# Optimization experiments

Measured on AMD Instinct MI355X. Metric: run time of the kernel, lower is better.

The kernel has to match this reference:

```python
import jax, jax.numpy as jnp
import numpy as np
import math

B, T, Dm, H = 512, 64, 1024, 16
dh = Dm // H
CD, SD = 32, 256  # smolgen compress_dim, shared_dim
SCALE = 1.0 / math.sqrt(dh)
RES_SCALE = 1.0 / math.sqrt(2.0)  # n_layers=1
EPS = 1e-5


def _ln(v, g, b):
    m = jnp.mean(v, axis=-1, keepdims=True)
    var = jnp.mean(jnp.square(v - m), axis=-1, keepdims=True)
    return (v - m) * jax.lax.rsqrt(var + EPS) * g + b


def setup_inputs() -> dict:
    key = jax.random.key(0)
    ks = jax.random.split(key, 16)
    s = 0.02
    return {
        "x": jax.random.normal(ks[0], (B, T, Dm), jnp.float32),
        # weights stored (in, out); y = x @ W + b
        "Wq": jax.random.normal(ks[1], (Dm, Dm), jnp.float32) * s,
        "Wk": jax.random.normal(ks[2], (Dm, Dm), jnp.float32) * s,
        "Wv": jax.random.normal(ks[3], (Dm, Dm), jnp.float32) * s,
        "Wo_w": jax.random.normal(ks[4], (Dm, Dm), jnp.float32) * s,
        "Wo_b": jnp.zeros((Dm,), jnp.float32),
        "static_bias": jax.random.normal(ks[5], (H, T, T), jnp.float32) * s,
        "aQ": jax.random.normal(ks[6], (H, T, T, dh), jnp.float32) * s,
        "aK": jax.random.normal(ks[7], (H, T, T, dh), jnp.float32) * s,
        "aV": jax.random.normal(ks[8], (H, T, T, dh), jnp.float32) * s,
        # Smolgen params
        "pt_w": jax.random.normal(ks[9], (Dm, CD), jnp.float32) * s,
        "pt_b": jnp.zeros((CD,), jnp.float32),
        "pg_w": jax.random.normal(ks[10], (T * CD, SD), jnp.float32) * s,
        "pg_b": jnp.zeros((SD,), jnp.float32),
        "ph_w": jax.random.normal(ks[11], (SD, H * SD), jnp.float32) * s,
        "ph_b": jnp.zeros((H * SD,), jnp.float32),
        "ln1_g": jnp.ones((SD,), jnp.float32),
        "ln1_b": jnp.zeros((SD,), jnp.float32),
        "ln2_g": jnp.ones((SD,), jnp.float32),
        "ln2_b": jnp.zeros((SD,), jnp.float32),
        "shared_w": jax.random.normal(ks[12], (SD, T * T), jnp.float32) * s,
    }


def _smolgen(x, pt_w, pt_b, pg_w, pg_b, ph_w, ph_b, ln1_g, ln1_b, ln2_g, ln2_b, shared_w):
    z = x @ pt_w + pt_b                      # (B,T,CD)
    g = z.reshape(x.shape[0], T * CD) @ pg_w + pg_b  # (B,SD)
    g = _ln(jax.nn.silu(g), ln1_g, ln1_b)
    u = g @ ph_w + ph_b                      # (B,H*SD)
    u = jax.nn.silu(u).reshape(-1, H, SD)
    u = _ln(u, ln2_g, ln2_b)
    return (u @ shared_w).reshape(-1, H, T, T)


def reference(x, Wq, Wk, Wv, Wo_w, Wo_b, static_bias, aQ, aK, aV,
              pt_w, pt_b, pg_w, pg_b, ph_w, ph_b,
              ln1_g, ln1_b, ln2_g, ln2_b, shared_w):
    Bx = x.shape[0]
    Q = (x @ Wq).reshape(Bx, T, H, dh).transpose(0, 2, 1, 3)  # (B,H,T,dh)
    K = (x @ Wk).reshape(Bx, T, H, dh).transpose(0, 2, 1, 3)
    V = (x @ Wv).reshape(Bx, T, H, dh).transpose(0, 2, 1, 3)
    logits = jnp.einsum('bhtd,bhsd->bhts', Q, K) * SCALE
    logits = logits + static_bias[None]
    logits = logits + jnp.einsum('bhtd,htsd->bhts', Q, aK) * SCALE
    logits = logits + jnp.einsum('htsd,bhsd->bhts', aQ, K) * SCALE
    logits = logits + (jnp.einsum('htsd,htsd->hts', aQ, aK) * SCALE)[None]
    logits = logits + _smolgen(x, pt_w, pt_b, pg_w, pg_b, ph_w, ph_b,
                               ln1_g, ln1_b, ln2_g, ln2_b, shared_w)
    attn = jax.nn.softmax(logits, axis=-1)  # dropout = identity (eval mode)
    out = jnp.einsum('bhts,bhsd->bhtd', attn, V)
    out = out + jnp.einsum('bhts,htsd->bhtd', attn, aV)
    out = out.transpose(0, 2, 1, 3).reshape(Bx, T, Dm)
    return (out @ Wo_w + Wo_b) * RES_SCALE
```

## Files before the change

### kernel.cpp

```cpp
#include <hip/hip_runtime.h>
#include <cstdint>
#include <cstdio>

typedef unsigned short u16;
typedef __attribute__((ext_vector_type(8))) short s8v;
typedef __attribute__((ext_vector_type(4))) float f4v;
typedef __attribute__((ext_vector_type(4))) unsigned short u16x4;
typedef const __attribute__((address_space(1))) void* gas_p;
typedef __attribute__((address_space(3))) void* las_p;

#define DEV __device__ __forceinline__

static constexpr float SCALE_ = 0.125f;
static constexpr float RES_SCALE_ = 0.7071067811865475f;
static constexpr float EPS_ = 1e-5f;

DEV u16 f2bf(float f) {
  uint32_t u = __float_as_uint(f);
  u += 0x7fffu + ((u >> 16) & 1u);
  return (u16)(u >> 16);
}
DEV float bf2f(u16 h) { return __uint_as_float(((uint32_t)h) << 16); }

DEV f4v mfma16(s8v a, s8v b, f4v c) {
  return __builtin_amdgcn_mfma_f32_16x16x32_bf16(a, b, c, 0, 0, 0);
}

#define WAITVM4 asm volatile("s_waitcnt vmcnt(4)" ::: "memory")
#define WAITVM0 asm volatile("s_waitcnt vmcnt(0)" ::: "memory")
#define SCHEDB  __builtin_amdgcn_sched_barrier(0)
#define BAR     __builtin_amdgcn_s_barrier()


__global__ void k_zero(float* __restrict__ p, long n) {
  long i = (long)blockIdx.x * blockDim.x + threadIdx.x;
  long stride = (long)gridDim.x * blockDim.x;
  for (; i < n; i += stride) p[i] = 0.f;
}

__global__ void k_cvt(const float* __restrict__ in, u16* __restrict__ out, long n4) {
  long i = (long)blockIdx.x * blockDim.x + threadIdx.x;
  long stride = (long)gridDim.x * blockDim.x;
  for (; i < n4; i += stride) {
    f4v v = *(const f4v*)&in[i * 4];
    u16x4 o;
    o.x = f2bf(v.x); o.y = f2bf(v.y); o.z = f2bf(v.z); o.w = f2bf(v.w);
    *(u16x4*)&out[i * 4] = o;
  }
}

__global__ void k_transpose(const float* __restrict__ in, u16* __restrict__ out, int K, int N) {
  __shared__ float tile[64][65];
  int kb = blockIdx.x * 64, nb = blockIdx.y * 64;
  for (int i = threadIdx.x; i < 4096; i += 256) {
    int r = i >> 6, c = i & 63;
    tile[r][c] = in[(long)(kb + r) * N + nb + c];
  }
  __syncthreads();
  for (int i = threadIdx.x; i < 4096; i += 256) {
    int c = i >> 6, r = i & 63;
    out[(long)(nb + c) * K + kb + r] = f2bf(tile[r][c]);
  }
}

__global__ void k_ptwt(const float* __restrict__ in, u16* __restrict__ out) {
  int idx = blockIdx.x * 256 + threadIdx.x;
  int n = idx >> 10, k = idx & 1023;
  out[idx] = f2bf(in[k * 32 + n]);
}

__global__ void k_avt(const float* __restrict__ aV, u16* __restrict__ aVt) {
  __shared__ float tile[64][65];
  int ht = blockIdx.x;
  const float* src = aV + (long)ht * 4096;
  for (int i = threadIdx.x; i < 4096; i += 256) {
    int s = i >> 6, d = i & 63;
    tile[s][d] = src[i];
  }
  __syncthreads();
  u16* dst = aVt + (long)ht * 4096;
  for (int i = threadIdx.x; i < 4096; i += 256) {
    int d = i >> 6, s = i & 63;
    dst[i] = f2bf(tile[s][d]);
  }
}

__global__ void k_extra(const float* __restrict__ sb, const float* __restrict__ aQ,
                        const float* __restrict__ aK, float* __restrict__ extra) {
  int idx = blockIdx.x * 256 + threadIdx.x;
  const float* q = aQ + (long)idx * 64;
  const float* k = aK + (long)idx * 64;
  float acc = 0.f;
#pragma unroll 8
  for (int d = 0; d < 64; d++) acc += q[d] * k[d];
  extra[idx] = sb[idx] + acc * SCALE_;
}

template <int EPI>
__launch_bounds__(512)
__global__ void k_gemm256(const u16* __restrict__ A, const u16* __restrict__ Bt,
                          void* __restrict__ Cv, const float* __restrict__ aux,
                          int M, int N, int K) {
  __shared__ u16 lds[65536];

  const int nwg = gridDim.x;
  int wg = blockIdx.x;
  if ((nwg & 7) == 0) wg = (wg & 7) * (nwg >> 3) + (wg >> 3);
  const int ntiles = N >> 8;
  const int mt = wg / ntiles, ntb = wg % ntiles;

  const int tid = threadIdx.x;
  const int lane = tid & 63, w = tid >> 6;
  const int wrB = (w >> 2) * 128, wcB = (w & 3) * 64;
  const int lr = lane & 15, lg = lane >> 4;
  const int hA = w >> 2;
  const int hB = (w & 3) >> 1;
  const int rB0 = (w & 1) * 64;
  const int xs0 = ((lg) ^ (lr & 7)) << 3;
  const int xs1 = ((4 + lg) ^ (lr & 7)) << 3;
  const int nt = K >> 6;

  const int sr = tid >> 3;
  const int sslot = (tid & 7) ^ (sr & 7);

  const u16* aSrc = A + (long)(mt * 256 + sr) * K + sslot * 8;
  const u16* bSrc = Bt + (long)(ntb * 256 + sr) * K + sslot * 8;
  const long h128 = (long)128 * K;
  const long r64 = (long)64 * K;

#define GLOADA(tile, h)                                                          \
  do {                                                                           \
    const int bu_ = (tile) & 1;                                                  \
    const long o_ = (long)(tile) * 64 + (h) * h128;                              \
    __builtin_amdgcn_global_load_lds((gas_p)(aSrc + o_), (las_p)&lds[(bu_ * 2 + (h)) * 8192 + w * 512], 16, 0, 0); \
    __builtin_amdgcn_global_load_lds((gas_p)(aSrc + o_ + r64), (las_p)&lds[(bu_ * 2 + (h)) * 8192 + 4096 + w * 512], 16, 0, 0); \
  } while (0)

#define GLOADB(tile, h)                                                          \
  do {                                                                           \
    const int bu_ = (tile) & 1;                                                  \
    const long o_ = (long)(tile) * 64 + (h) * h128;                              \
    __builtin_amdgcn_global_load_lds((gas_p)(bSrc + o_), (las_p)&lds[32768 + (bu_ * 2 + (h)) * 8192 + w * 512], 16, 0, 0); \
    __builtin_amdgcn_global_load_lds((gas_p)(bSrc + o_ + r64), (las_p)&lds[32768 + (bu_ * 2 + (h)) * 8192 + 4096 + w * 512], 16, 0, 0); \
  } while (0)

  f4v acc[8][4];
#pragma unroll
  for (int mi = 0; mi < 8; mi++)
#pragma unroll
    for (int ni = 0; ni < 4; ni++) acc[mi][ni] = (f4v){0.f, 0.f, 0.f, 0.f};

  GLOADA(0, 0); GLOADA(0, 1);
  GLOADB(0, 0); GLOADB(0, 1);
  {
    const int t1 = (nt > 1) ? 1 : 0;
    GLOADB(t1, 0); GLOADB(t1, 1);
  }
  WAITVM0;
  BAR;

  s8v AF[4][2], b01[2][2], b23[2][2];

  {
    const int aB0 = hA * 8192;
    const int bB0 = 32768 + hB * 8192;
#pragma unroll
    for (int mi = 0; mi < 4; mi++) {
      const int ro = (mi * 16 + lr) * 64;
      AF[mi][0] = *(const s8v*)&lds[aB0 + ro + xs0];
      AF[mi][1] = *(const s8v*)&lds[aB0 + ro + xs1];
    }
#pragma unroll
    for (int ni = 0; ni < 2; ni++) {
      const int ro = (rB0 + ni * 16 + lr) * 64;
      b01[ni][0] = *(const s8v*)&lds[bB0 + ro + xs0];
      b01[ni][1] = *(const s8v*)&lds[bB0 + ro + xs1];
    }
  }
  SCHEDB;

  for (int t = 0; t < nt; ++t) {
    const int p = t & 1, q = p ^ 1;
    const int aN = (t + 1 < nt) ? t + 1 : nt - 1;
    const int bN = (t + 2 < nt) ? t + 2 : nt - 1;
    const int aBase = (p * 2 + hA) * 8192;
    const int bBase = 32768 + (p * 2 + hB) * 8192;
    const int aBaseN = (q * 2 + hA) * 8192;
    const int bBaseN = 32768 + (q * 2 + hB) * 8192;

#pragma unroll
    for (int ni = 0; ni < 2; ni++) {
      const int ro = (rB0 + (2 + ni) * 16 + lr) * 64;
      b23[ni][0] = *(const s8v*)&lds[bBase + ro + xs0];
      b23[ni][1] = *(const s8v*)&lds[bBase + ro + xs1];
    }
    SCHEDB;
    GLOADA(aN, 0);
    BAR;
    __builtin_amdgcn_s_setprio(1);
#pragma unroll
    for (int mi = 0; mi < 4; mi++)
#pragma unroll
      for (int ks = 0; ks < 2; ks++)
#pragma unroll
        for (int ni = 0; ni < 2; ni++)
          acc[mi][ni] = mfma16(AF[mi][ks], b01[ni][ks], acc[mi][ni]);
    __builtin_amdgcn_s_setprio(0);
    BAR;

    GLOADA(aN, 1);
    BAR;
    __builtin_amdgcn_s_setprio(1);
#pragma unroll
    for (int mi = 0; mi < 4; mi++) {
#pragma unroll
      for (int ks = 0; ks < 2; ks++)
#pragma unroll
        for (int ni = 0; ni < 2; ni++)
          acc[mi][2 + ni] = mfma16(AF[mi][ks], b23[ni][ks], acc[mi][2 + ni]);
      const int ro = (64 + mi * 16 + lr) * 64;
      AF[mi][0] = *(const s8v*)&lds[aBase + ro + xs0];
      AF[mi][1] = *(const s8v*)&lds[aBase + ro + xs1];
      SCHEDB;
    }
    __builtin_amdgcn_s_setprio(0);
    BAR;

    GLOADB(bN, 0);
    BAR;
    __builtin_amdgcn_s_setprio(1);
#pragma unroll
    for (int mi = 0; mi < 4; mi++)
#pragma unroll
      for (int ks = 0; ks < 2; ks++)
#pragma unroll
        for (int ni = 0; ni < 2; ni++)
          acc[4 + mi][ni] = mfma16(AF[mi][ks], b01[ni][ks], acc[4 + mi][ni]);
    __builtin_amdgcn_s_setprio(0);
    BAR;

    GLOADB(bN, 1);
    WAITVM4;
    BAR;
#pragma unroll
    for (int ni = 0; ni < 2; ni++) {
      const int ro = (rB0 + ni * 16 + lr) * 64;
      b01[ni][0] = *(const s8v*)&lds[bBaseN + ro + xs0];
      b01[ni][1] = *(const s8v*)&lds[bBaseN + ro + xs1];
    }
    SCHEDB;
    __builtin_amdgcn_s_setprio(1);
#pragma unroll
    for (int mi = 0; mi < 4; mi++) {
#pragma unroll
      for (int ks = 0; ks < 2; ks++)
#pragma unroll
        for (int ni = 0; ni < 2; ni++)
          acc[4 + mi][2 + ni] = mfma16(AF[mi][ks], b23[ni][ks], acc[4 + mi][2 + ni]);
      const int ro = (mi * 16 + lr) * 64;
      AF[mi][0] = *(const s8v*)&lds[aBaseN + ro + xs0];
      AF[mi][1] = *(const s8v*)&lds[aBaseN + ro + xs1];
      SCHEDB;
    }
    __builtin_amdgcn_s_setprio(0);
    BAR;
  }
#undef GLOADA
#undef GLOADB

  const int rbase = mt * 256 + wrB + lg * 4;
  const int cbase = ntb * 256 + wcB + lr;
  if (EPI == 0) {
    u16* C = (u16*)Cv;
#pragma unroll
    for (int mi = 0; mi < 8; mi++)
#pragma unroll
      for (int ni = 0; ni < 4; ni++)
#pragma unroll
        for (int j = 0; j < 4; j++)
          C[(long)(rbase + mi * 16 + j) * N + (cbase + ni * 16)] = f2bf(acc[mi][ni][j]);
  } else {
    float* C = (float*)Cv;
#pragma unroll
    for (int mi = 0; mi < 8; mi++)
#pragma unroll
      for (int ni = 0; ni < 4; ni++)
#pragma unroll
        for (int j = 0; j < 4; j++) {
          const int col = cbase + ni * 16;
          C[(long)(rbase + mi * 16 + j) * N + col] =
              (acc[mi][ni][j] + aux[col]) * RES_SCALE_;
        }
  }
}

template <int EPI>
__launch_bounds__(256)
__global__ void k_gemm(const u16* __restrict__ A, const u16* __restrict__ Bt,
                       void* __restrict__ Cv, const float* __restrict__ aux,
                       int M, int N, int K) {
  __shared__ u16 As[4096];
  __shared__ u16 Bs[4096];
  const int ntiles = N >> 7;
  const int mt = blockIdx.x / ntiles;
  const int nt = blockIdx.x % ntiles;
  const int tid = threadIdx.x;
  const int lane = tid & 63;
  const int w = tid >> 6;
  const int wr = w >> 1, wc = w & 1;
  const int lr = lane & 15, lg = lane >> 4;

  f4v acc[4][4];
#pragma unroll
  for (int m = 0; m < 4; m++)
#pragma unroll
    for (int n = 0; n < 4; n++) acc[m][n] = (f4v){0.f, 0.f, 0.f, 0.f};

  const u16* aSrc = A + (long)(mt * 128 + (tid >> 2)) * K + ((tid & 3) << 3);
  const u16* bSrc = Bt + (long)(nt * 128 + (tid >> 2)) * K + ((tid & 3) << 3);
  const long rowStep = (long)64 * K;

  const int kIters = K >> 5;
  for (int kb = 0; kb < kIters; kb++) {
    if (kb) __syncthreads();
    const u16* aP = aSrc + (kb << 5);
    const u16* bP = bSrc + (kb << 5);
    __builtin_amdgcn_global_load_lds((gas_p)aP, (las_p)&As[w * 512], 16, 0, 0);
    __builtin_amdgcn_global_load_lds((gas_p)(aP + rowStep), (las_p)&As[2048 + w * 512], 16, 0, 0);
    __builtin_amdgcn_global_load_lds((gas_p)bP, (las_p)&Bs[w * 512], 16, 0, 0);
    __builtin_amdgcn_global_load_lds((gas_p)(bP + rowStep), (las_p)&Bs[2048 + w * 512], 16, 0, 0);
    WAITVM0;
    __syncthreads();

    s8v af[4];
#pragma unroll
    for (int m = 0; m < 4; m++)
      af[m] = *(const s8v*)&As[(wr * 64 + m * 16 + lr) * 32 + (lg << 3)];
#pragma unroll
    for (int n = 0; n < 4; n++) {
      s8v bf = *(const s8v*)&Bs[(wc * 64 + n * 16 + lr) * 32 + (lg << 3)];
#pragma unroll
      for (int m = 0; m < 4; m++) acc[m][n] = mfma16(af[m], bf, acc[m][n]);
    }
  }

  const int rbase = mt * 128 + wr * 64 + lg * 4;
  const int cbase = nt * 128 + wc * 64 + lr;
  if (EPI == 1) {
    float* C = (float*)Cv;
#pragma unroll
    for (int m = 0; m < 4; m++)
#pragma unroll
      for (int n = 0; n < 4; n++)
#pragma unroll
        for (int j = 0; j < 4; j++) {
          int row = rbase + m * 16 + j;
          int col = cbase + n * 16;
          C[(long)row * N + col] = acc[m][n][j] + aux[col];
        }
  } else {
    u16* C = (u16*)Cv;
#pragma unroll
    for (int m = 0; m < 4; m++)
#pragma unroll
      for (int n = 0; n < 4; n++)
#pragma unroll
        for (int j = 0; j < 4; j++) {
          int row = rbase + m * 16 + j;
          int col = cbase + n * 16;
          C[(long)row * N + col] = f2bf(acc[m][n][j] + aux[((row & 15) << 12) | col]);
        }
  }
}


__launch_bounds__(256)
__global__ void k_smola_gemm(const u16* __restrict__ xbf, const u16* __restrict__ ptwT,
                             const float* __restrict__ ptb, u16* __restrict__ z) {
  const int rt = blockIdx.x;
  const int w = threadIdx.x >> 6, lane = threadIdx.x & 63;
  const int lr = lane & 15, lg = lane >> 4;
  const int row0 = rt * 64 + w * 16;
  f4v acc[2];
  acc[0] = (f4v){0.f, 0.f, 0.f, 0.f};
  acc[1] = (f4v){0.f, 0.f, 0.f, 0.f};
  const u16* aBase = xbf + (long)(row0 + lr) * 1024;
  const u16* bBase = ptwT + (long)lr * 1024;
#pragma unroll 4
  for (int k0 = 0; k0 < 1024; k0 += 32) {
    s8v a = *(const s8v*)&aBase[k0 + (lg << 3)];
#pragma unroll
    for (int n = 0; n < 2; n++) {
      s8v b = *(const s8v*)&bBase[(long)(n << 4) * 1024 + k0 + (lg << 3)];
      acc[n] = mfma16(a, b, acc[n]);
    }
  }
#pragma unroll
  for (int n = 0; n < 2; n++)
#pragma unroll
    for (int j = 0; j < 4; j++) {
      int col = (n << 4) + lr;
      z[(long)(row0 + lg * 4 + j) * 32 + col] = f2bf(acc[n][j] + ptb[col]);
    }
}

__launch_bounds__(64)
__global__ void k_smolb_gemm(const u16* __restrict__ z, const u16* __restrict__ pgwT,
                             const float* __restrict__ pgb, float* __restrict__ out) {
  const int bid = blockIdx.x;
  const int rt = bid >> 2, ct = bid & 3;
  const int lane = threadIdx.x;
  const int lr = lane & 15, lg = lane >> 4;
  f4v acc[4];
#pragma unroll
  for (int n = 0; n < 4; n++) acc[n] = (f4v){0.f, 0.f, 0.f, 0.f};
  const u16* aBase = z + (long)(rt * 16 + lr) * 2048;
  const u16* bBase = pgwT + (long)(ct * 64 + lr) * 2048;
#pragma unroll 4
  for (int k0 = 0; k0 < 2048; k0 += 32) {
    s8v a = *(const s8v*)&aBase[k0 + (lg << 3)];
#pragma unroll
    for (int n = 0; n < 4; n++) {
      s8v b = *(const s8v*)&bBase[(long)(n << 4) * 2048 + k0 + (lg << 3)];
      acc[n] = mfma16(a, b, acc[n]);
    }
  }
#pragma unroll
  for (int n = 0; n < 4; n++)
#pragma unroll
    for (int j = 0; j < 4; j++) {
      int row = rt * 16 + lg * 4 + j;
      int col = ct * 64 + (n << 4) + lr;
      out[(long)row * 256 + col] = acc[n][j] + pgb[col];
    }
}

__launch_bounds__(64)
__global__ void k_ln2(const float* __restrict__ uraw, const float* __restrict__ g2,
                      const float* __restrict__ b2, u16* __restrict__ ubf) {
  const int row = blockIdx.x;
  const int lane = threadIdx.x;
  f4v x = *(const f4v*)&uraw[(long)row * 256 + lane * 4];
  float v[4];
  float s = 0.f, q = 0.f;
#pragma unroll
  for (int j = 0; j < 4; j++) {
    float xx = x[j];
    v[j] = xx / (1.f + __expf(-xx));
    s += v[j]; q += v[j] * v[j];
  }
#pragma unroll
  for (int mk = 1; mk < 64; mk <<= 1) { s += __shfl_xor(s, mk); q += __shfl_xor(q, mk); }
  float mean = s * (1.f / 256.f);
  float var = q * (1.f / 256.f) - mean * mean;
  float rs = rsqrtf(var + EPS_);
  u16x4 o;
  float o0 = (v[0] - mean) * rs * g2[lane * 4 + 0] + b2[lane * 4 + 0];
  float o1 = (v[1] - mean) * rs * g2[lane * 4 + 1] + b2[lane * 4 + 1];
  float o2 = (v[2] - mean) * rs * g2[lane * 4 + 2] + b2[lane * 4 + 2];
  float o3 = (v[3] - mean) * rs * g2[lane * 4 + 3] + b2[lane * 4 + 3];
  o.x = f2bf(o0); o.y = f2bf(o1); o.z = f2bf(o2); o.w = f2bf(o3);
  *(u16x4*)&ubf[(long)row * 256 + lane * 4] = o;
}


__launch_bounds__(64)
__global__ void k_l2(const u16* __restrict__ qkv, const u16* __restrict__ aKb,
                     u16* __restrict__ l2b) {
  const int bid = blockIdx.x;
  const int bt = bid & 7, t = (bid >> 3) & 63, h = bid >> 9;
  const int lane = threadIdx.x;
  const int lr = lane & 15, lg = lane >> 4;
  f4v acc[4][4];
#pragma unroll
  for (int m = 0; m < 4; m++)
#pragma unroll
    for (int n = 0; n < 4; n++) acc[m][n] = (f4v){0.f, 0.f, 0.f, 0.f};
  const u16* qb = qkv + (long)t * 3072 + h * 64;
  const u16* kb = aKb + ((long)h * 64 + t) * 4096;
#pragma unroll
  for (int ks = 0; ks < 2; ks++) {
    s8v a[4], bb[4];
#pragma unroll
    for (int m = 0; m < 4; m++) {
      int brow = bt * 64 + m * 16 + lr;
      a[m] = *(const s8v*)&qb[(long)brow * 196608 + ks * 32 + (lg << 3)];
    }
#pragma unroll
    for (int n = 0; n < 4; n++)
      bb[n] = *(const s8v*)&kb[(n * 16 + lr) * 64 + ks * 32 + (lg << 3)];
#pragma unroll
    for (int m = 0; m < 4; m++)
#pragma unroll
      for (int n = 0; n < 4; n++) acc[m][n] = mfma16(a[m], bb[n], acc[m][n]);
  }
  u16* dst = l2b + ((long)h * 64 + t) * 32768;
#pragma unroll
  for (int m = 0; m < 4; m++)
#pragma unroll
    for (int n = 0; n < 4; n++)
#pragma unroll
      for (int j = 0; j < 4; j++) {
        int brow = bt * 64 + m * 16 + lg * 4 + j;
        int s = n * 16 + lr;
        dst[(long)brow * 64 + s] = f2bf(SCALE_ * acc[m][n][j]);
      }
}

__launch_bounds__(64)
__global__ void k_l3(const u16* __restrict__ qkv, const u16* __restrict__ aQb,
                     u16* __restrict__ l3a) {
  const int bid = blockIdx.x;
  const int bt = bid & 7, s = (bid >> 3) & 63, h = bid >> 9;
  const int lane = threadIdx.x;
  const int lr = lane & 15, lg = lane >> 4;
  f4v acc[4][4];
#pragma unroll
  for (int m = 0; m < 4; m++)
#pragma unroll
    for (int n = 0; n < 4; n++) acc[m][n] = (f4v){0.f, 0.f, 0.f, 0.f};
  const u16* kb = qkv + (long)s * 3072 + 1024 + h * 64;
  const u16* qb = aQb + (long)h * 262144 + (long)s * 64;
#pragma unroll
  for (int ks = 0; ks < 2; ks++) {
    s8v a[4], bb[4];
#pragma unroll
    for (int m = 0; m < 4; m++) {
      int brow = bt * 64 + m * 16 + lr;
      a[m] = *(const s8v*)&kb[(long)brow * 196608 + ks * 32 + (lg << 3)];
    }
#pragma unroll
    for (int n = 0; n < 4; n++) {
      int tc = n * 16 + lr;
      bb[n] = *(const s8v*)&qb[(long)tc * 4096 + ks * 32 + (lg << 3)];
    }
#pragma unroll
    for (int m = 0; m < 4; m++)
#pragma unroll
      for (int n = 0; n < 4; n++) acc[m][n] = mfma16(a[m], bb[n], acc[m][n]);
  }
#pragma unroll
  for (int m = 0; m < 4; m++)
#pragma unroll
    for (int n = 0; n < 4; n++)
#pragma unroll
      for (int j = 0; j < 4; j++) {
        int brow = bt * 64 + m * 16 + lg * 4 + j;
        int tc = n * 16 + lr;
        long idx = (((long)brow * 16 + h) * 64 + s) * 64 + tc;
        l3a[idx] = f2bf(SCALE_ * acc[m][n][j]);
      }
}

__launch_bounds__(64)
__global__ void k_c(const u16* __restrict__ attnb, const u16* __restrict__ aVt,
                    u16* __restrict__ outh) {
  const int bid = blockIdx.x;
  const int bt = bid & 7, t = (bid >> 3) & 63, h = bid >> 9;
  const int lane = threadIdx.x;
  const int lr = lane & 15, lg = lane >> 4;
  f4v acc[4][4];
#pragma unroll
  for (int m = 0; m < 4; m++)
#pragma unroll
    for (int n = 0; n < 4; n++) acc[m][n] = (f4v){0.f, 0.f, 0.f, 0.f};
  const u16* ab = attnb + ((long)h * 64 + t) * 64;
  const u16* vb = aVt + ((long)h * 64 + t) * 4096;
#pragma unroll
  for (int ks = 0; ks < 2; ks++) {
    s8v a[4], bb[4];
#pragma unroll
    for (int m = 0; m < 4; m++) {
      int brow = bt * 64 + m * 16 + lr;
      a[m] = *(const s8v*)&ab[(long)brow * 65536 + ks * 32 + (lg << 3)];
    }
#pragma unroll
    for (int n = 0; n < 4; n++)
      bb[n] = *(const s8v*)&vb[(n * 16 + lr) * 64 + ks * 32 + (lg << 3)];
#pragma unroll
    for (int m = 0; m < 4; m++)
#pragma unroll
      for (int n = 0; n < 4; n++) acc[m][n] = mfma16(a[m], bb[n], acc[m][n]);
  }
#pragma unroll
  for (int m = 0; m < 4; m++)
#pragma unroll
    for (int n = 0; n < 4; n++)
#pragma unroll
      for (int j = 0; j < 4; j++) {
        int brow = bt * 64 + m * 16 + lg * 4 + j;
        int d = n * 16 + lr;
        long idx = ((long)brow * 64 + t) * 1024 + h * 64 + d;
        outh[idx] = f2bf(bf2f(outh[idx]) + acc[m][n][j]);
      }
}

__launch_bounds__(256)
__global__ void k_attn(const u16* __restrict__ qkv, const u16* __restrict__ logits,
                       const u16* __restrict__ l2b, u16* __restrict__ l3a,
                       u16* __restrict__ outh) {
  __shared__ u16 Qs[64 * 72];
  __shared__ u16 Ks[64 * 72];
  __shared__ u16 Vt[64 * 72];
  __shared__ u16 Ps[64 * 72];
  const int bh = blockIdx.x;
  const int b = bh >> 4, h = bh & 15;
  const int tid = threadIdx.x;
  const int lane = tid & 63, w = tid >> 6;
  const int lr = lane & 15, lg = lane >> 4;
  const u16* qbase = qkv + (long)b * 196608 + h * 64;

#pragma unroll
  for (int c = 0; c < 2; c++) {
    int flat = c * 2048 + tid * 8;
    int row = flat >> 6, k = flat & 63;
    const u16* src = &qbase[(long)row * 3072 + k];
    *(s8v*)&Qs[row * 72 + k] = *(const s8v*)(src);
    *(s8v*)&Ks[row * 72 + k] = *(const s8v*)(src + 1024);
    s8v v = *(const s8v*)(src + 2048);
#pragma unroll
    for (int j = 0; j < 8; j++) Vt[(k + j) * 72 + row] = (u16)v[j];
  }
  __syncthreads();

  f4v sacc[4];
#pragma unroll
  for (int n = 0; n < 4; n++) sacc[n] = (f4v){0.f, 0.f, 0.f, 0.f};
#pragma unroll
  for (int ks = 0; ks < 2; ks++) {
    s8v a = *(const s8v*)&Qs[(w * 16 + lr) * 72 + ks * 32 + (lg << 3)];
#pragma unroll
    for (int n = 0; n < 4; n++) {
      s8v bb = *(const s8v*)&Ks[(n * 16 + lr) * 72 + ks * 32 + (lg << 3)];
      sacc[n] = mfma16(a, bb, sacc[n]);
    }
  }

  const long base = (long)bh * 4096;
  const int r0 = w * 16 + lg * 4;
  float p[4][4];
#pragma unroll
  for (int n = 0; n < 4; n++) {
    int s = n * 16 + lr;
    u16x4 l3v = *(const u16x4*)&l3a[base + s * 64 + r0];
#pragma unroll
    for (int j = 0; j < 4; j++) {
      float l3f = bf2f(((const u16*)&l3v)[j]);
      float l2f = bf2f(l2b[(((long)h * 64 + r0 + j) * 512 + b) * 64 + s]);
      float lgf = bf2f(logits[base + (r0 + j) * 64 + s]);
      p[n][j] = sacc[n][j] * SCALE_ + lgf + l3f + l2f;
    }
  }
#pragma unroll
  for (int j = 0; j < 4; j++) {
    float m = fmaxf(fmaxf(p[0][j], p[1][j]), fmaxf(p[2][j], p[3][j]));
    m = fmaxf(m, __shfl_xor(m, 1));
    m = fmaxf(m, __shfl_xor(m, 2));
    m = fmaxf(m, __shfl_xor(m, 4));
    m = fmaxf(m, __shfl_xor(m, 8));
    float s0 = 0.f;
#pragma unroll
    for (int n = 0; n < 4; n++) { p[n][j] = __expf(p[n][j] - m); s0 += p[n][j]; }
    s0 += __shfl_xor(s0, 1);
    s0 += __shfl_xor(s0, 2);
    s0 += __shfl_xor(s0, 4);
    s0 += __shfl_xor(s0, 8);
    float inv = 1.f / s0;
#pragma unroll
    for (int n = 0; n < 4; n++) p[n][j] *= inv;
  }

  __syncthreads();

#pragma unroll
  for (int n = 0; n < 4; n++) {
    int s = n * 16 + lr;
#pragma unroll
    for (int j = 0; j < 4; j++) {
      u16 pb = f2bf(p[n][j]);
      l3a[base + (r0 + j) * 64 + s] = pb;
      Ps[(r0 + j) * 72 + s] = pb;
    }
  }
  __syncthreads();

  f4v oacc[4];
#pragma unroll
  for (int n = 0; n < 4; n++) oacc[n] = (f4v){0.f, 0.f, 0.f, 0.f};
#pragma unroll
  for (int ks = 0; ks < 2; ks++) {
    s8v a = *(const s8v*)&Ps[(w * 16 + lr) * 72 + ks * 32 + (lg << 3)];
#pragma unroll
    for (int n = 0; n < 4; n++) {
      s8v vb = *(const s8v*)&Vt[(n * 16 + lr) * 72 + ks * 32 + (lg << 3)];
      oacc[n] = mfma16(a, vb, oacc[n]);
    }
  }
  u16* obase = outh + (long)b * 65536 + h * 64;
#pragma unroll
  for (int n = 0; n < 4; n++)
#pragma unroll
    for (int j = 0; j < 4; j++)
      obase[(long)(r0 + j) * 1024 + n * 16 + lr] = f2bf(oacc[n][j]);
}


extern "C" void kernel_launch(void* const* d_in, const int* in_sizes, int n_in,
                              void* d_out, int out_size, void* d_ws, size_t ws_size,
                              hipStream_t stream) {
  (void)in_sizes; (void)n_in;
  const float* x    = (const float*)d_in[0];
  const float* Wq   = (const float*)d_in[1];
  const float* Wk   = (const float*)d_in[2];
  const float* Wv   = (const float*)d_in[3];
  const float* Wo_w = (const float*)d_in[4];
  const float* Wo_b = (const float*)d_in[5];
  const float* sb   = (const float*)d_in[6];
  const float* aQ   = (const float*)d_in[7];
  const float* aK   = (const float*)d_in[8];
  const float* aV   = (const float*)d_in[9];
  const float* pt_w = (const float*)d_in[10];
  const float* pt_b = (const float*)d_in[11];
  const float* pg_w = (const float*)d_in[12];
  const float* pg_b = (const float*)d_in[13];
  const float* ph_w = (const float*)d_in[14];
  const float* ph_b = (const float*)d_in[15];
  const float* ln1g = (const float*)d_in[16];
  const float* ln1b = (const float*)d_in[17];
  const float* ln2g = (const float*)d_in[18];
  const float* ln2b = (const float*)d_in[19];
  const float* shw  = (const float*)d_in[20];

  char* wsp = (char*)d_ws;
  size_t off = 0;
  auto alloc = [&](size_t bytes) {
    void* p = wsp + off;
    off += (bytes + 255) & ~(size_t)255;
    return p;
  };
  u16*   xbf    = (u16*)alloc(33554432ull * 2);
  u16*   qkv    = (u16*)alloc(100663296ull * 2);
  u16*   logits = (u16*)alloc(33554432ull * 2);
  u16*   l3a    = (u16*)alloc(33554432ull * 2);
  u16*   l2b    = (u16*)alloc(33554432ull * 2);
  u16*   Wqkvt  = (u16*)alloc(3145728ull * 2);
  u16*   Wot    = (u16*)alloc(1048576ull * 2);
  u16*   phwt   = (u16*)alloc(1048576ull * 2);
  u16*   swt    = (u16*)alloc(1048576ull * 2);
  u16*   aKb    = (u16*)alloc(4194304ull * 2);
  u16*   aQb    = (u16*)alloc(4194304ull * 2);
  u16*   aVt    = (u16*)alloc(4194304ull * 2);
  float* extra  = (float*)alloc(65536ull * 4);
  u16*   z      = (u16*)alloc(1048576ull * 2);
  u16*   g      = (u16*)alloc(131072ull * 2);
  float* uraw   = (float*)alloc(2097152ull * 4);
  u16*   ubf    = (u16*)alloc(2097152ull * 2);
  u16*   ptwT   = (u16*)alloc(32768ull * 2);
  u16*   pgwT   = (u16*)alloc(524288ull * 2);
  float* uraw2  = (float*)alloc(131072ull * 4);
  u16*   outh   = xbf;
  float* dout   = (float*)d_out;

  if (off > ws_size) {
    fprintf(stderr, "[kernel_launch] insufficient workspace: need %zu have %zu\n",
            off, ws_size);
    k_zero<<<2048, 256, 0, stream>>>(dout, (long)out_size);
    return;
  }

  k_cvt<<<2048, 256, 0, stream>>>(x, xbf, 8388608);
  k_transpose<<<dim3(16, 16), 256, 0, stream>>>(Wq, Wqkvt, 1024, 1024);
  k_transpose<<<dim3(16, 16), 256, 0, stream>>>(Wk, Wqkvt + 1048576, 1024, 1024);
  k_transpose<<<dim3(16, 16), 256, 0, stream>>>(Wv, Wqkvt + 2097152, 1024, 1024);
  k_transpose<<<dim3(16, 16), 256, 0, stream>>>(Wo_w, Wot, 1024, 1024);
  k_transpose<<<dim3(4, 64), 256, 0, stream>>>(ph_w, phwt, 256, 4096);
  k_transpose<<<dim3(4, 64), 256, 0, stream>>>(shw, swt, 256, 4096);
  k_transpose<<<dim3(32, 4), 256, 0, stream>>>(pg_w, pgwT, 2048, 256);
  k_ptwt<<<128, 256, 0, stream>>>(pt_w, ptwT);
  k_cvt<<<2048, 256, 0, stream>>>(aK, aKb, 1048576);
  k_cvt<<<2048, 256, 0, stream>>>(aQ, aQb, 1048576);
  k_avt<<<1024, 256, 0, stream>>>(aV, aVt);
  k_extra<<<256, 256, 0, stream>>>(sb, aQ, aK, extra);

  k_gemm256<0><<<1536, 512, 0, stream>>>(xbf, Wqkvt, qkv, nullptr, 32768, 3072, 1024);

  k_smola_gemm<<<512, 256, 0, stream>>>(xbf, ptwT, pt_b, z);
  k_smolb_gemm<<<128, 64, 0, stream>>>(z, pgwT, pg_b, uraw2);
  k_ln2<<<512, 64, 0, stream>>>(uraw2, ln1g, ln1b, g);
  k_gemm<1><<<128, 256, 0, stream>>>(g, phwt, uraw, ph_b, 512, 4096, 256);
  k_ln2<<<8192, 64, 0, stream>>>(uraw, ln2g, ln2b, ubf);
  k_gemm<2><<<2048, 256, 0, stream>>>(ubf, swt, logits, extra, 8192, 4096, 256);

  k_l2<<<8192, 64, 0, stream>>>(qkv, aKb, l2b);
  k_l3<<<8192, 64, 0, stream>>>(qkv, aQb, l3a);
  k_attn<<<8192, 256, 0, stream>>>(qkv, logits, l2b, l3a, outh);
  k_c<<<8192, 64, 0, stream>>>(l3a, aVt, outh);
  k_gemm256<3><<<512, 512, 0, stream>>>(outh, Wot, dout, Wo_b, 32768, 1024, 1024);
}
```

Before: 767.3 us.

## Fuse prep kernels into one launch, merge l2/l3, drop GEMM barriers

```diff
diff --git a/kernel.cpp b/kernel.cpp
--- a/kernel.cpp
+++ b/kernel.cpp
@@ -38,9 +38,11 @@
   for (; i < n; i += stride) p[i] = 0.f;
 }
 
-__global__ void k_cvt(const float* __restrict__ in, u16* __restrict__ out, long n4) {
-  long i = (long)blockIdx.x * blockDim.x + threadIdx.x;
-  long stride = (long)gridDim.x * blockDim.x;
+
+DEV void dev_cvt(const float* __restrict__ in, u16* __restrict__ out, long n4,
+                 int bid, int nblocks) {
+  long i = (long)bid * 256 + threadIdx.x;
+  long stride = (long)nblocks * 256;
   for (; i < n4; i += stride) {
     f4v v = *(const f4v*)&in[i * 4];
     u16x4 o;
@@ -49,9 +51,9 @@
   }
 }
 
-__global__ void k_transpose(const float* __restrict__ in, u16* __restrict__ out, int K, int N) {
-  __shared__ float tile[64][65];
-  int kb = blockIdx.x * 64, nb = blockIdx.y * 64;
+DEV void dev_transpose(const float* __restrict__ in, u16* __restrict__ out,
+                       int K, int N, int bx, int by, float tile[64][65]) {
+  int kb = bx * 64, nb = by * 64;
   for (int i = threadIdx.x; i < 4096; i += 256) {
     int r = i >> 6, c = i & 63;
     tile[r][c] = in[(long)(kb + r) * N + nb + c];
@@ -63,15 +65,8 @@
   }
 }
 
-__global__ void k_ptwt(const float* __restrict__ in, u16* __restrict__ out) {
-  int idx = blockIdx.x * 256 + threadIdx.x;
-  int n = idx >> 10, k = idx & 1023;
-  out[idx] = f2bf(in[k * 32 + n]);
-}
-
-__global__ void k_avt(const float* __restrict__ aV, u16* __restrict__ aVt) {
-  __shared__ float tile[64][65];
-  int ht = blockIdx.x;
+DEV void dev_avt(const float* __restrict__ aV, u16* __restrict__ aVt, int ht,
+                 float tile[64][65]) {
   const float* src = aV + (long)ht * 4096;
   for (int i = threadIdx.x; i < 4096; i += 256) {
     int s = i >> 6, d = i & 63;
@@ -85,15 +80,60 @@
   }
 }
 
-__global__ void k_extra(const float* __restrict__ sb, const float* __restrict__ aQ,
-                        const float* __restrict__ aK, float* __restrict__ extra) {
-  int idx = blockIdx.x * 256 + threadIdx.x;
-  const float* q = aQ + (long)idx * 64;
-  const float* k = aK + (long)idx * 64;
-  float acc = 0.f;
+__launch_bounds__(256)
+__global__ void k_prep(const float* __restrict__ x, u16* __restrict__ xbf,
+                       const float* __restrict__ Wq, const float* __restrict__ Wk,
+                       const float* __restrict__ Wv, const float* __restrict__ Wo,
+                       u16* __restrict__ Wqkvt, u16* __restrict__ Wot,
+                       const float* __restrict__ ph_w, u16* __restrict__ phwt,
+                       const float* __restrict__ shw, u16* __restrict__ swt,
+                       const float* __restrict__ pg_w, u16* __restrict__ pgwT,
+                       const float* __restrict__ pt_w, u16* __restrict__ ptwT,
+                       const float* __restrict__ aK, u16* __restrict__ aKb,
+                       const float* __restrict__ aQ, u16* __restrict__ aQb,
+                       const float* __restrict__ aV, u16* __restrict__ aVt,
+                       const float* __restrict__ sb, float* __restrict__ extra) {
+  __shared__ float tile[64][65];
+  int b = blockIdx.x;
+  if (b < 2048) { dev_cvt(x, xbf, 8388608, b, 2048); return; }
+  b -= 2048;
+  if (b < 1024) {
+    const float* src = (b < 256) ? Wq : (b < 512) ? Wk : (b < 768) ? Wv : Wo;
+    u16* dst = (b < 256) ? Wqkvt : (b < 512) ? (Wqkvt + 1048576)
+             : (b < 768) ? (Wqkvt + 2097152) : Wot;
+    int id = b & 255;
+    dev_transpose(src, dst, 1024, 1024, id & 15, id >> 4, tile);
+    return;
+  }
+  b -= 1024;
+  if (b < 256) { dev_transpose(ph_w, phwt, 256, 4096, b & 3, b >> 2, tile); return; }
+  b -= 256;
+  if (b < 256) { dev_transpose(shw, swt, 256, 4096, b & 3, b >> 2, tile); return; }
+  b -= 256;
+  if (b < 128) { dev_transpose(pg_w, pgwT, 2048, 256, b & 31, b >> 5, tile); return; }
+  b -= 128;
+  if (b < 128) {
+    int idx = b * 256 + threadIdx.x;
+    int n = idx >> 10, k = idx & 1023;
+    ptwT[idx] = f2bf(pt_w[k * 32 + n]);
+    return;
+  }
+  b -= 128;
+  if (b < 512) { dev_cvt(aK, aKb, 1048576, b, 512); return; }
+  b -= 512;
+  if (b < 512) { dev_cvt(aQ, aQb, 1048576, b, 512); return; }
+  b -= 512;
+  if (b < 1024) { dev_avt(aV, aVt, b, tile); return; }
+  b -= 1024;
+  {
+    int idx = b * 256 + threadIdx.x;
+    const float* q = aQ + (long)idx * 64;
+    const float* k = aK + (long)idx * 64;
+    float acc = 0.f;
 #pragma unroll 8
-  for (int d = 0; d < 64; d++) acc += q[d] * k[d];
-  extra[idx] = sb[idx] + acc * SCALE_;
+    for (int d = 0; d < 64; d++) acc += q[d] * k[d];
+    extra[idx] = sb[idx] + acc * SCALE_;
+  }
 }
 
 template <int EPI>
@@ -206,7 +246,6 @@
         for (int ni = 0; ni < 2; ni++)
           acc[mi][ni] = mfma16(AF[mi][ks], b01[ni][ks], acc[mi][ni]);
     __builtin_amdgcn_s_setprio(0);
-    BAR;
 
     GLOADA(aN, 1);
     BAR;
@@ -237,7 +276,6 @@
         for (int ni = 0; ni < 2; ni++)
           acc[4 + mi][ni] = mfma16(AF[mi][ks], b01[ni][ks], acc[4 + mi][ni]);
     __builtin_amdgcn_s_setprio(0);
-    BAR;
 
     GLOADB(bN, 1);
     WAITVM4;
@@ -263,7 +301,6 @@
       SCHEDB;
     }
     __builtin_amdgcn_s_setprio(0);
-    BAR;
   }
 #undef GLOADA
 #undef GLOADB
@@ -465,10 +502,9 @@
 
 
 __launch_bounds__(64)
-__global__ void k_l2(const u16* __restrict__ qkv, const u16* __restrict__ aKb,
-                     u16* __restrict__ l2b) {
-  const int bid = blockIdx.x;
-  const int bt = bid & 7, t = (bid >> 3) & 63, h = bid >> 9;
+__global__ void k_l23(const u16* __restrict__ qkv, const u16* __restrict__ aKb,
+                      const u16* __restrict__ aQb, u16* __restrict__ l2b,
+                      u16* __restrict__ l3a) {
   const int lane = threadIdx.x;
   const int lr = lane & 15, lg = lane >> 4;
   f4v acc[4][4];
@@ -476,80 +512,74 @@
   for (int m = 0; m < 4; m++)
 #pragma unroll
     for (int n = 0; n < 4; n++) acc[m][n] = (f4v){0.f, 0.f, 0.f, 0.f};
-  const u16* qb = qkv + (long)t * 3072 + h * 64;
-  const u16* kb = aKb + ((long)h * 64 + t) * 4096;
-#pragma unroll
-  for (int ks = 0; ks < 2; ks++) {
-    s8v a[4], bb[4];
-#pragma unroll
-    for (int m = 0; m < 4; m++) {
-      int brow = bt * 64 + m * 16 + lr;
-      a[m] = *(const s8v*)&qb[(long)brow * 196608 + ks * 32 + (lg << 3)];
-    }
-#pragma unroll
-    for (int n = 0; n < 4; n++)
-      bb[n] = *(const s8v*)&kb[(n * 16 + lr) * 64 + ks * 32 + (lg << 3)];
+
+  if (blockIdx.x < 8192) {
+    const int bid = blockIdx.x;
+    const int bt = bid & 7, t = (bid >> 3) & 63, h = bid >> 9;
+    const u16* qb = qkv + (long)t * 3072 + h * 64;
+    const u16* kb = aKb + ((long)h * 64 + t) * 4096;
+#pragma unroll
+    for (int ks = 0; ks < 2; ks++) {
+      s8v a[4], bb[4];
+#pragma unroll
+      for (int m = 0; m < 4; m++) {
+        int brow = bt * 64 + m * 16 + lr;
+        a[m] = *(const s8v*)&qb[(long)brow * 196608 + ks * 32 + (lg << 3)];
+      }
+#pragma unroll
+      for (int n = 0; n < 4; n++)
+        bb[n] = *(const s8v*)&kb[(n * 16 + lr) * 64 + ks * 32 + (lg << 3)];
+#pragma unroll
+      for (int m = 0; m < 4; m++)
+#pragma unroll
+        for (int n = 0; n < 4; n++) acc[m][n] = mfma16(a[m], bb[n], acc[m][n]);
+    }
+    u16* dst = l2b + ((long)h * 64 + t) * 32768;
 #pragma unroll
     for (int m = 0; m < 4; m++)
 #pragma unroll
-      for (int n = 0; n < 4; n++) acc[m][n] = mfma16(a[m], bb[n], acc[m][n]);
-  }
-  u16* dst = l2b + ((long)h * 64 + t) * 32768;
-#pragma unroll
-  for (int m = 0; m < 4; m++)
-#pragma unroll
-    for (int n = 0; n < 4; n++)
-#pragma unroll
-      for (int j = 0; j < 4; j++) {
-        int brow = bt * 64 + m * 16 + lg * 4 + j;
-        int s = n * 16 + lr;
-        dst[(long)brow * 64 + s] = f2bf(SCALE_ * acc[m][n][j]);
+      for (int n = 0; n < 4; n++)
+#pragma unroll
+        for (int j = 0; j < 4; j++) {
+          int brow = bt * 64 + m * 16 + lg * 4 + j;
+          int s = n * 16 + lr;
+          dst[(long)brow * 64 + s] = f2bf(SCALE_ * acc[m][n][j]);
+        }
+  } else {
+    const int bid = blockIdx.x - 8192;
+    const int bt = bid & 7, s = (bid >> 3) & 63, h = bid >> 9;
+    const u16* kb = qkv + (long)s * 3072 + 1024 + h * 64;
+    const u16* qb = aQb + (long)h * 262144 + (long)s * 64;
+#pragma unroll
+    for (int ks = 0; ks < 2; ks++) {
+      s8v a[4], bb[4];
+#pragma unroll
+      for (int m = 0; m < 4; m++) {
+        int brow = bt * 64 + m * 16 + lr;
+        a[m] = *(const s8v*)&kb[(long)brow * 196608 + ks * 32 + (lg << 3)];
       }
-}
-
-__launch_bounds__(64)
-__global__ void k_l3(const u16* __restrict__ qkv, const u16* __restrict__ aQb,
-                     u16* __restrict__ l3a) {
-  const int bid = blockIdx.x;
-  const int bt = bid & 7, s = (bid >> 3) & 63, h = bid >> 9;
-  const int lane = threadIdx.x;
-  const int lr = lane & 15, lg = lane >> 4;
-  f4v acc[4][4];
-#pragma unroll
-  for (int m = 0; m < 4; m++)
-#pragma unroll
-    for (int n = 0; n < 4; n++) acc[m][n] = (f4v){0.f, 0.f, 0.f, 0.f};
-  const u16* kb = qkv + (long)s * 3072 + 1024 + h * 64;
-  const u16* qb = aQb + (long)h * 262144 + (long)s * 64;
-#pragma unroll
-  for (int ks = 0; ks < 2; ks++) {
-    s8v a[4], bb[4];
-#pragma unroll
-    for (int m = 0; m < 4; m++) {
-      int brow = bt * 64 + m * 16 + lr;
-      a[m] = *(const s8v*)&kb[(long)brow * 196608 + ks * 32 + (lg << 3)];
-    }
-#pragma unroll
-    for (int n = 0; n < 4; n++) {
-      int tc = n * 16 + lr;
-      bb[n] = *(const s8v*)&qb[(long)tc * 4096 + ks * 32 + (lg << 3)];
+#pragma unroll
+      for (int n = 0; n < 4; n++) {
+        int tc = n * 16 + lr;
+        bb[n] = *(const s8v*)&qb[(long)tc * 4096 + ks * 32 + (lg << 3)];
+      }
+#pragma unroll
+      for (int m = 0; m < 4; m++)
+#pragma unroll
+        for (int n = 0; n < 4; n++) acc[m][n] = mfma16(a[m], bb[n], acc[m][n]);
     }
 #pragma unroll
     for (int m = 0; m < 4; m++)
 #pragma unroll
-      for (int n = 0; n < 4; n++) acc[m][n] = mfma16(a[m], bb[n], acc[m][n]);
-  }
-#pragma unroll
-  for (int m = 0; m < 4; m++)
-#pragma unroll
-    for (int n = 0; n < 4; n++)
-#pragma unroll
-      for (int j = 0; j < 4; j++) {
-        int brow = bt * 64 + m * 16 + lg * 4 + j;
-        int tc = n * 16 + lr;
-        long idx = (((long)brow * 16 + h) * 64 + s) * 64 + tc;
-        l3a[idx] = f2bf(SCALE_ * acc[m][n][j]);
-      }
+      for (int n = 0; n < 4; n++)
+#pragma unroll
+        for (int j = 0; j < 4; j++) {
+          int brow = bt * 64 + m * 16 + lg * 4 + j;
+          int tc = n * 16 + lr;
+          long idx = (((long)brow * 16 + h) * 64 + s) * 64 + tc;
+          l3a[idx] = f2bf(SCALE_ * acc[m][n][j]);
+        }
+  }
 }
 
 __launch_bounds__(64)
@@ -768,19 +798,9 @@
     return;
   }
 
-  k_cvt<<<2048, 256, 0, stream>>>(x, xbf, 8388608);
-  k_transpose<<<dim3(16, 16), 256, 0, stream>>>(Wq, Wqkvt, 1024, 1024);
-  k_transpose<<<dim3(16, 16), 256, 0, stream>>>(Wk, Wqkvt + 1048576, 1024, 1024);
-  k_transpose<<<dim3(16, 16), 256, 0, stream>>>(Wv, Wqkvt + 2097152, 1024, 1024);
-  k_transpose<<<dim3(16, 16), 256, 0, stream>>>(Wo_w, Wot, 1024, 1024);
-  k_transpose<<<dim3(4, 64), 256, 0, stream>>>(ph_w, phwt, 256, 4096);
-  k_transpose<<<dim3(4, 64), 256, 0, stream>>>(shw, swt, 256, 4096);
-  k_transpose<<<dim3(32, 4), 256, 0, stream>>>(pg_w, pgwT, 2048, 256);
-  k_ptwt<<<128, 256, 0, stream>>>(pt_w, ptwT);
-  k_cvt<<<2048, 256, 0, stream>>>(aK, aKb, 1048576);
-  k_cvt<<<2048, 256, 0, stream>>>(aQ, aQb, 1048576);
-  k_avt<<<1024, 256, 0, stream>>>(aV, aVt);
-  k_extra<<<256, 256, 0, stream>>>(sb, aQ, aK, extra);
+  k_prep<<<6144, 256, 0, stream>>>(x, xbf, Wq, Wk, Wv, Wo_w, Wqkvt, Wot,
+                                   ph_w, phwt, shw, swt, pg_w, pgwT, pt_w, ptwT,
+                                   aK, aKb, aQ, aQb, aV, aVt, sb, extra);
 
   k_gemm256<0><<<1536, 512, 0, stream>>>(xbf, Wqkvt, qkv, nullptr, 32768, 3072, 1024);
 
@@ -791,8 +811,7 @@
   k_ln2<<<8192, 64, 0, stream>>>(uraw, ln2g, ln2b, ubf);
   k_gemm<2><<<2048, 256, 0, stream>>>(ubf, swt, logits, extra, 8192, 4096, 256);
 
-  k_l2<<<8192, 64, 0, stream>>>(qkv, aKb, l2b);
-  k_l3<<<8192, 64, 0, stream>>>(qkv, aQb, l3a);
+  k_l23<<<16384, 64, 0, stream>>>(qkv, aKb, aQb, l2b, l3a);
   k_attn<<<8192, 256, 0, stream>>>(qkv, logits, l2b, l3a, outh);
   k_c<<<8192, 64, 0, stream>>>(l3a, aVt, outh);
   k_gemm256<3><<<512, 512, 0, stream>>>(outh, Wot, dout, Wo_b, 32768, 1024, 1024);
```

After: 728.1 us. -5.1%, faster.
